# Kernel tuning notes

Hardware: AMD Instinct MI355X
Metric: run time of the kernel (lower is better)

## Reference

```python
import jax, jax.numpy as jnp
import numpy as np

B, N, DIM = 1, 65536, 256
H, D, G = 8, 64, 64  # heads, dim_head, slice_num


def setup_inputs() -> dict:
    key = jax.random.key(0)
    ks = jax.random.split(key, 16)
    s = 0.02
    return {
        "x": jax.random.normal(ks[0], (B, N, DIM), jnp.float32),
        "Wx": jax.random.normal(ks[1], (H * D, DIM), jnp.float32) * s,
        "bx": jnp.zeros((H * D,), jnp.float32),
        "Wt1": jax.random.normal(ks[2], (G, D), jnp.float32) * s,
        "bt1": jnp.zeros((G,), jnp.float32),
        "Wt2": jax.random.normal(ks[3], (1, G), jnp.float32) * s,
        "bt2": jnp.zeros((1,), jnp.float32),
        "bias": jnp.ones((1, H, 1, 1), jnp.float32) * 0.5,
        "Ws": jax.random.normal(ks[4], (G, D), jnp.float32) * s,
        "bs": jnp.zeros((G,), jnp.float32),
        "Wq": jax.random.normal(ks[5], (D, D), jnp.float32) * s,
        "Wk": jax.random.normal(ks[6], (D, D), jnp.float32) * s,
        "Wv": jax.random.normal(ks[7], (D, D), jnp.float32) * s,
        "Wout": jax.random.normal(ks[8], (DIM, H * D), jnp.float32) * s,
        "bout": jnp.zeros((DIM,), jnp.float32),
        "u": jax.random.uniform(ks[9], (B, H, N, G), jnp.float32),
    }


def _gelu(t):
    return jax.nn.gelu(t, approximate=False)  # torch default exact GELU


def reference(x, Wx, bx, Wt1, bt1, Wt2, bt2, bias, Ws, bs, Wq, Wk, Wv, Wout, bout, u):
    b, n, _ = x.shape
    h, d, g = Wt1.shape[1] and bias.shape[1], Wq.shape[0], Ws.shape[0]
    # project and split heads: b n (h d) -> b h n d
    x_mid = (x @ Wx.T + bx).reshape(b, n, h, d).transpose(0, 2, 1, 3)
    # per-point temperature MLP + learned bias, clamped
    temp = _gelu(_gelu(x_mid @ Wt1.T + bt1) @ Wt2.T + bt2) + bias  # (b,h,n,1)
    temp = jnp.maximum(temp, 0.01)
    # gumbel-softmax slice routing (soft, hard=False)
    logits = x_mid @ Ws.T + bs  # (b,h,n,g)
    gnoise = -jnp.log(-jnp.log(u + 1e-8) + 1e-8)
    slice_weights = jax.nn.softmax((logits + gnoise) / temp, axis=-1)
    norm = slice_weights.sum(axis=2)  # (b,h,g)
    # gather-aggregate points into g slice tokens
    slice_tokens = jnp.einsum('bhnc,bhng->bhgc', x_mid, slice_weights)
    slice_tokens = slice_tokens / (norm[..., None] + 1e-5)
    # tiny g x g attention among slice tokens
    q = slice_tokens @ Wq.T
    k = slice_tokens @ Wk.T
    v = slice_tokens @ Wv.T
    attn = jax.nn.softmax((q @ k.transpose(0, 1, 3, 2)) * (d ** -0.5), axis=-1)
    out_slice = attn @ v  # (b,h,g,d)
    # scatter-combine back to points
    out = jnp.einsum('bhgd,bhng->bhnd', out_slice, slice_weights)
    out = out.transpose(0, 2, 1, 3).reshape(b, n, h * d)
    return out @ Wout.T + bout
```

## Files before the change

kernel.cpp:

```cpp
#include <hip/hip_runtime.h>
#include <math.h>

#define NPTS  65536
#define DIMX  256
#define NH    8
#define HDIM  512

typedef __attribute__((ext_vector_type(4))) float f32x4;
typedef __attribute__((ext_vector_type(8))) short short8;
typedef __attribute__((ext_vector_type(8))) unsigned short ushort8;
typedef __attribute__((ext_vector_type(4))) unsigned short us4;

__device__ __forceinline__ ushort f2bf(float f) {
    unsigned x = __float_as_uint(f);
    return (ushort)((x + 0x7fffu + ((x >> 16) & 1u)) >> 16);
}
__device__ __forceinline__ float bf2f(ushort u) {
    return __uint_as_float((unsigned)u << 16);
}
__device__ __forceinline__ float erf_fast(float x) {
    float ax = fabsf(x);
    float t  = __builtin_amdgcn_rcpf(1.0f + 0.3275911f * ax);
    float p  = fmaf(fmaf(fmaf(fmaf(1.061405429f, t, -1.453152027f), t,
                   1.421413741f), t, -0.284496736f), t, 0.254829592f) * t;
    float y  = 1.0f - p * __expf(-ax * ax);
    return copysignf(y, x);
}
__device__ __forceinline__ float gelu_fast(float x) {
    return 0.5f * x * (1.0f + erf_fast(x * 0.7071067811865476f));
}

__global__ __launch_bounds__(256)
void prep_wb_kernel(const float* __restrict__ Ws, const float* __restrict__ Wt1,
                    ushort* __restrict__ wb) {
    const int t = threadIdx.x;
    #pragma unroll
    for (int i = 0; i < 32; ++i) {
        int idx = i * 256 + t;
        int row = idx >> 6, col = idx & 63;
        float v = (row < 64) ? Ws[row * 64 + col] : Wt1[(row - 64) * 64 + col];
        wb[idx] = f2bf(v);
    }
}

__global__ __launch_bounds__(256)
void gemm_xmid_kernel(const float* __restrict__ A, const float* __restrict__ B,
                      const float* __restrict__ bias, ushort* __restrict__ C) {
    __shared__ __align__(16) ushort Al[128][64];
    __shared__ __align__(16) ushort Bl[128][64];
    const int m0 = blockIdx.x * 128, n0 = blockIdx.y * 128;
    const int t = threadIdx.x, l = t & 63, w = t >> 6;
    const int wr = w >> 1, wc = w & 1;
    const int lr = l & 15, lq = l >> 4;

    f32x4 acc[4][4];
    #pragma unroll
    for (int mi = 0; mi < 4; ++mi)
        #pragma unroll
        for (int ni = 0; ni < 4; ++ni) acc[mi][ni] = (f32x4){0.f, 0.f, 0.f, 0.f};

    for (int ks = 0; ks < 4; ++ks) {
        __syncthreads();
        #pragma unroll
        for (int i = 0; i < 4; ++i) {
            int idx = i * 256 + t;
            int row = idx >> 3, g = idx & 7;
            const float* ap = &A[(size_t)(m0 + row) * 256 + ks * 64 + g * 8];
            float4 a0 = *(const float4*)ap;
            float4 a1 = *(const float4*)(ap + 4);
            ushort8 av = { f2bf(a0.x), f2bf(a0.y), f2bf(a0.z), f2bf(a0.w),
                           f2bf(a1.x), f2bf(a1.y), f2bf(a1.z), f2bf(a1.w) };
            *(ushort8*)&Al[row][(g ^ (row & 7)) * 8] = av;
            const float* bp = &B[(size_t)(n0 + row) * 256 + ks * 64 + g * 8];
            float4 b0 = *(const float4*)bp;
            float4 b1 = *(const float4*)(bp + 4);
            ushort8 bv = { f2bf(b0.x), f2bf(b0.y), f2bf(b0.z), f2bf(b0.w),
                           f2bf(b1.x), f2bf(b1.y), f2bf(b1.z), f2bf(b1.w) };
            *(ushort8*)&Bl[row][(g ^ (row & 7)) * 8] = bv;
        }
        __syncthreads();
        #pragma unroll
        for (int kf = 0; kf < 2; ++kf) {
            short8 af[4], bfr[4];
            #pragma unroll
            for (int mi = 0; mi < 4; ++mi) {
                int row = wr * 64 + mi * 16 + lr, g = kf * 4 + lq;
                af[mi] = *(const short8*)&Al[row][(g ^ (row & 7)) * 8];
            }
            #pragma unroll
            for (int ni = 0; ni < 4; ++ni) {
                int row = wc * 64 + ni * 16 + lr, g = kf * 4 + lq;
                bfr[ni] = *(const short8*)&Bl[row][(g ^ (row & 7)) * 8];
            }
            #pragma unroll
            for (int mi = 0; mi < 4; ++mi)
                #pragma unroll
                for (int ni = 0; ni < 4; ++ni)
                    acc[mi][ni] = __builtin_amdgcn_mfma_f32_16x16x32_bf16(
                        af[mi], bfr[ni], acc[mi][ni], 0, 0, 0);
        }
    }
    #pragma unroll
    for (int ni = 0; ni < 4; ++ni) {
        int col = n0 + wc * 64 + ni * 16 + lr;
        float bb = bias[col];
        #pragma unroll
        for (int mi = 0; mi < 4; ++mi)
            #pragma unroll
            for (int j = 0; j < 4; ++j) {
                int row = m0 + wr * 64 + mi * 16 + lq * 4 + j;
                C[(size_t)row * 512 + col] = f2bf(acc[mi][ni][j] + bb);
            }
    }
}

__global__ __launch_bounds__(256)
void lgt1_mfma_kernel(const ushort* __restrict__ xmb,
                      const ushort* __restrict__ wb,
                      const float* __restrict__ bs,  const float* __restrict__ bt1,
                      const float* __restrict__ Wt2, const float* __restrict__ bt2,
                      const float* __restrict__ biasp,
                      const float* __restrict__ u,
                      ushort* __restrict__ swb) {
    __shared__ __align__(16) ushort Al[128][64];
    const int h = blockIdx.y, m0 = blockIdx.x * 128;
    const int t = threadIdx.x, l = t & 63, w = t >> 6;
    const int lr = l & 15, lq = l >> 4;
    const float LOG2E = 1.4426950408889634f;
    const float LN2   = 0.6931471805599453f;
    const float SH2   = 36.0673760222f;

    #pragma unroll
    for (int i = 0; i < 4; ++i) {
        int idx = i * 256 + t;
        int row = idx >> 3, g = idx & 7;
        ushort8 av = *(const ushort8*)&xmb[(size_t)(m0 + row) * 512 + h * 64 + g * 8];
        *(ushort8*)&Al[row][(g ^ (row & 7)) * 8] = av;
    }

    float uu0[4][4];
    #pragma unroll
    for (int jj = 0; jj < 4; ++jj) {
        const int n = m0 + w * 32 + lq * 4 + jj;
        const float* up = &u[((size_t)h * NPTS + n) * 64 + lr];
        #pragma unroll
        for (int ni = 0; ni < 4; ++ni) uu0[jj][ni] = up[ni * 16];
    }
    __syncthreads();

    f32x4 acc[2][8];
    #pragma unroll
    for (int mi = 0; mi < 2; ++mi)
        #pragma unroll
        for (int ni = 0; ni < 8; ++ni) acc[mi][ni] = (f32x4){0.f, 0.f, 0.f, 0.f};

    #pragma unroll
    for (int kf = 0; kf < 2; ++kf) {
        const int g = kf * 4 + lq;
        short8 af[2], bfr[8];
        #pragma unroll
        for (int mi = 0; mi < 2; ++mi) {
            int row = w * 32 + mi * 16 + lr;
            af[mi] = *(const short8*)&Al[row][(g ^ (row & 7)) * 8];
        }
        #pragma unroll
        for (int ni = 0; ni < 8; ++ni)
            bfr[ni] = *(const short8*)&wb[(size_t)(ni * 16 + lr) * 64 + g * 8];
        #pragma unroll
        for (int mi = 0; mi < 2; ++mi)
            #pragma unroll
            for (int ni = 0; ni < 8; ++ni)
                acc[mi][ni] = __builtin_amdgcn_mfma_f32_16x16x32_bf16(
                    af[mi], bfr[ni], acc[mi][ni], 0, 0, 0);
    }

    float uu1[4][4];
    #pragma unroll
    for (int jj = 0; jj < 4; ++jj) {
        const int n = m0 + w * 32 + 16 + lq * 4 + jj;
        const float* up = &u[((size_t)h * NPTS + n) * 64 + lr];
        #pragma unroll
        for (int ni = 0; ni < 4; ++ni) uu1[jj][ni] = up[ni * 16];
    }

    const float bt2v = bt2[0], biasph = biasp[h];
    float bsr[4], bt1r[4], wt2r[4];
    #pragma unroll
    for (int ni = 0; ni < 4; ++ni) {
        bsr[ni]  = bs [ni * 16 + lr];
        bt1r[ni] = bt1[ni * 16 + lr];
        wt2r[ni] = Wt2[ni * 16 + lr];
    }

    #pragma unroll
    for (int mi = 0; mi < 2; ++mi) {
        float ts[4];
        #pragma unroll
        for (int jj = 0; jj < 4; ++jj) {
            float s = 0.f;
            #pragma unroll
            for (int ni = 0; ni < 4; ++ni)
                s += gelu_fast(acc[mi][ni + 4][jj] + bt1r[ni]) * wt2r[ni];
            ts[jj] = s;
        }
        #pragma unroll
        for (int off = 1; off <= 8; off <<= 1) {
            #pragma unroll
            for (int jj = 0; jj < 4; ++jj) ts[jj] += __shfl_xor(ts[jj], off);
        }
        float invt[4], invt2[4];
        #pragma unroll
        for (int jj = 0; jj < 4; ++jj) {
            float tmp = gelu_fast(ts[jj] + bt2v) + biasph;
            tmp = fmaxf(tmp, 0.01f);
            invt[jj]  = __builtin_amdgcn_rcpf(tmp);
            invt2[jj] = invt[jj] * LOG2E;
        }
        float sv[4][4], ps[4] = {0.f, 0.f, 0.f, 0.f};
        #pragma unroll
        for (int jj = 0; jj < 4; ++jj) {
            #pragma unroll
            for (int ni = 0; ni < 4; ++ni) {
                float uuv = (mi == 0 ? uu0[jj][ni] : uu1[jj][ni]);
                float L1 = __log2f(uuv + 1e-8f);
                float inner = fmaf(-LN2, L1, 1e-8f);
                float L2v = __log2f(inner);
                float base = fmaf(acc[mi][ni][jj] + bsr[ni], invt2[jj], -SH2);
                sv[jj][ni] = __builtin_amdgcn_exp2f(fmaf(-invt[jj], L2v, base));
                ps[jj] += sv[jj][ni];
            }
        }
        #pragma unroll
        for (int off = 1; off <= 8; off <<= 1) {
            #pragma unroll
            for (int jj = 0; jj < 4; ++jj) ps[jj] += __shfl_xor(ps[jj], off);
        }
        #pragma unroll
        for (int jj = 0; jj < 4; ++jj) {
            const int n = m0 + w * 32 + mi * 16 + lq * 4 + jj;
            const float inv = __builtin_amdgcn_rcpf(ps[jj]);
            ushort* sp = &swb[(size_t)n * 512 + h * 64 + lr];
            #pragma unroll
            for (int ni = 0; ni < 4; ++ni)
                sp[ni * 16] = f2bf(sv[jj][ni] * inv);
        }
    }
}

__global__ __launch_bounds__(256)
void gather_mfma_kernel(const ushort* __restrict__ xmb, const ushort* __restrict__ swb,
                        float* __restrict__ stp, float* __restrict__ normp) {
    __shared__ __align__(16) ushort swT[64][128];
    __shared__ __align__(16) ushort xT [64][128];
    const int h  = blockIdx.y;
    const int n0 = blockIdx.x * 1024;
    const int t  = threadIdx.x, l = t & 63, w = t >> 6;
    const int lr = l & 15, lq = l >> 4;
    const int gb = t & 7;
    const int ng = t >> 3;

    f32x4 acc[4][4];
    #pragma unroll
    for (int gi = 0; gi < 4; ++gi)
        #pragma unroll
        for (int ci = 0; ci < 4; ++ci) acc[gi][ci] = (f32x4){0.f, 0.f, 0.f, 0.f};
    float nrm8[8];
    #pragma unroll
    for (int j = 0; j < 8; ++j) nrm8[j] = 0.f;

    for (int r = 0; r < 8; ++r) {
        const int nt = n0 + r * 128;
        ushort8 sv[4], xv[4];
        #pragma unroll
        for (int i = 0; i < 4; ++i) {
            int n = nt + ng * 4 + i;
            sv[i] = *(const ushort8*)&swb[(size_t)n * 512 + h * 64 + gb * 8];
            xv[i] = *(const ushort8*)&xmb[(size_t)n * 512 + h * 64 + gb * 8];
        }
        __syncthreads();
        #pragma unroll
        for (int j = 0; j < 8; ++j) {
            int g   = gb * 8 + j;
            int swz = (ng >> 1) ^ (g & 7) ^ ((g >> 3) & 7);
            int off = swz * 8 + (ng & 1) * 4;
            us4 s4 = { sv[0][j], sv[1][j], sv[2][j], sv[3][j] };
            us4 x4 = { xv[0][j], xv[1][j], xv[2][j], xv[3][j] };
            *(us4*)&swT[g][off] = s4;
            *(us4*)&xT [g][off] = x4;
            nrm8[j] += (bf2f(sv[0][j]) + bf2f(sv[1][j]))
                     + (bf2f(sv[2][j]) + bf2f(sv[3][j]));
        }
        __syncthreads();
        short8 af[4], bfr[4];
        #pragma unroll
        for (int gi = 0; gi < 4; ++gi) {
            int g   = gi * 16 + lr;
            int swz = (w * 4 + lq) ^ (g & 7) ^ ((g >> 3) & 7);
            af[gi]  = *(const short8*)&swT[g][swz * 8];
            bfr[gi] = *(const short8*)&xT [g][swz * 8];
        }
        #pragma unroll
        for (int gi = 0; gi < 4; ++gi)
            #pragma unroll
            for (int ci = 0; ci < 4; ++ci)
                acc[gi][ci] = __builtin_amdgcn_mfma_f32_16x16x32_bf16(
                    af[gi], bfr[ci], acc[gi][ci], 0, 0, 0);
    }

    const size_t base = ((size_t)h * 256 + blockIdx.x * 4 + w) * 4096;
    #pragma unroll
    for (int gi = 0; gi < 4; ++gi)
        #pragma unroll
        for (int ci = 0; ci < 4; ++ci)
            #pragma unroll
            for (int j = 0; j < 4; ++j)
                stp[base + (size_t)(gi * 16 + lq * 4 + j) * 64 + ci * 16 + lr]
                    = acc[gi][ci][j];

    __syncthreads();
    float* narr = (float*)swT;
    #pragma unroll
    for (int j = 0; j < 8; ++j) narr[ng * 64 + gb * 8 + j] = nrm8[j];
    __syncthreads();
    if (t < 64) {
        float s = 0.f;
        #pragma unroll 8
        for (int k = 0; k < 32; ++k) s += narr[k * 64 + t];
        normp[((size_t)h * 64 + blockIdx.x) * 64 + t] = s;
    }
}

__global__ __launch_bounds__(256)
void reduce_st_kernel(const float* __restrict__ stp, const float* __restrict__ normp,
                      float* __restrict__ st_red, float* __restrict__ nrm) {
    const int h = blockIdx.x;
    const int e = blockIdx.y * 256 + threadIdx.x;
    float s = 0.f;
    #pragma unroll 8
    for (int ch = 0; ch < 256; ++ch)
        s += stp[((size_t)h * 256 + ch) * 4096 + e];
    st_red[(size_t)h * 4096 + e] = s;
    if (blockIdx.y == 0 && threadIdx.x < 64) {
        float ns = 0.f;
        #pragma unroll 8
        for (int ch = 0; ch < 64; ++ch)
            ns += normp[((size_t)h * 64 + ch) * 64 + threadIdx.x];
        nrm[h * 64 + threadIdx.x] = ns + 1e-5f;
    }
}

__global__ __launch_bounds__(256)
void attn_small_kernel(const float* __restrict__ st_red, const float* __restrict__ nrm,
                       const float* __restrict__ Wq, const float* __restrict__ Wk,
                       const float* __restrict__ Wv, float* __restrict__ osl) {
    __shared__ float st[64][68];
    __shared__ float ql[64][68];
    __shared__ float kl[64][68];
    __shared__ float vl[64][68];
    __shared__ float sc[64][68];
    __shared__ float nl[64];
    const int h = blockIdx.x;
    const int t = threadIdx.x;

    if (t < 64) nl[t] = nrm[h * 64 + t];
    __syncthreads();
    for (int e = t; e < 4096; e += 256)
        st[e>>6][e&63] = st_red[(size_t)h * 4096 + e] / nl[e>>6];
    __syncthreads();
    for (int e = t; e < 4096; e += 256) {
        int g = e >> 6, dd = e & 63;
        float aq = 0.f, ak = 0.f, av = 0.f;
        for (int cc = 0; cc < 64; ++cc) {
            float sv = st[g][cc];
            aq = fmaf(sv, Wq[dd*64 + cc], aq);
            ak = fmaf(sv, Wk[dd*64 + cc], ak);
            av = fmaf(sv, Wv[dd*64 + cc], av);
        }
        ql[g][dd] = aq; kl[g][dd] = ak; vl[g][dd] = av;
    }
    __syncthreads();
    for (int e = t; e < 4096; e += 256) {
        int g = e >> 6, gp = e & 63;
        float s = 0.f;
        for (int dd = 0; dd < 64; ++dd) s = fmaf(ql[g][dd], kl[gp][dd], s);
        sc[g][gp] = s * 0.125f;
    }
    __syncthreads();
    if (t < 64) {
        float m = -1e30f;
        for (int j = 0; j < 64; ++j) m = fmaxf(m, sc[t][j]);
        float ssum = 0.f;
        for (int j = 0; j < 64; ++j) { float p = expf(sc[t][j] - m); sc[t][j] = p; ssum += p; }
        float inv = 1.f / ssum;
        for (int j = 0; j < 64; ++j) sc[t][j] *= inv;
    }
    __syncthreads();
    for (int e = t; e < 4096; e += 256) {
        int g = e >> 6, dd = e & 63;
        float s = 0.f;
        for (int gp = 0; gp < 64; ++gp) s = fmaf(sc[g][gp], vl[gp][dd], s);
        osl[(size_t)h * 4096 + e] = s;
    }
}

__global__ __launch_bounds__(256)
void fold_kernel(const float* __restrict__ osl, const float* __restrict__ Wout,
                 float* __restrict__ Mt) {
    __shared__ float os[64][65];
    __shared__ float wl[128][65];
    const int h  = blockIdx.x;
    const int i0 = blockIdx.y * 128;
    const int t  = threadIdx.x;
    for (int e = t; e < 4096; e += 256) os[e>>6][e&63] = osl[(size_t)h * 4096 + e];
    for (int e = t; e < 8192; e += 256) {
        int i = e >> 6, d = e & 63;
        wl[i][d] = Wout[(size_t)(i0 + i) * HDIM + h * 64 + d];
    }
    __syncthreads();
    const int g = t & 63, iq = t >> 6;
    #pragma unroll 4
    for (int k = 0; k < 32; ++k) {
        int i = iq * 32 + k;
        float s = 0.f;
        #pragma unroll
        for (int d = 0; d < 64; ++d) s = fmaf(os[g][d], wl[i][d], s);
        Mt[(size_t)(i0 + i) * HDIM + h * 64 + g] = s;
    }
}

__global__ __launch_bounds__(256)
void gemm_out_kernel(const ushort* __restrict__ A, const float* __restrict__ B,
                     const float* __restrict__ bias, float* __restrict__ C) {
    __shared__ __align__(16) ushort Al[128][64];
    __shared__ __align__(16) ushort Bl[128][64];
    const int m0 = blockIdx.x * 128, n0 = blockIdx.y * 128;
    const int t = threadIdx.x, l = t & 63, w = t >> 6;
    const int wr = w >> 1, wc = w & 1;
    const int lr = l & 15, lq = l >> 4;

    f32x4 acc[4][4];
    #pragma unroll
    for (int mi = 0; mi < 4; ++mi)
        #pragma unroll
        for (int ni = 0; ni < 4; ++ni) acc[mi][ni] = (f32x4){0.f, 0.f, 0.f, 0.f};

    for (int ks = 0; ks < 8; ++ks) {
        __syncthreads();
        #pragma unroll
        for (int i = 0; i < 4; ++i) {
            int idx = i * 256 + t;
            int row = idx >> 3, g = idx & 7;
            ushort8 av = *(const ushort8*)&A[(size_t)(m0 + row) * 512 + ks * 64 + g * 8];
            *(ushort8*)&Al[row][(g ^ (row & 7)) * 8] = av;
            const float* bp = &B[(size_t)(n0 + row) * 512 + ks * 64 + g * 8];
            float4 b0 = *(const float4*)bp;
            float4 b1 = *(const float4*)(bp + 4);
            ushort8 bv = { f2bf(b0.x), f2bf(b0.y), f2bf(b0.z), f2bf(b0.w),
                           f2bf(b1.x), f2bf(b1.y), f2bf(b1.z), f2bf(b1.w) };
            *(ushort8*)&Bl[row][(g ^ (row & 7)) * 8] = bv;
        }
        __syncthreads();
        #pragma unroll
        for (int kf = 0; kf < 2; ++kf) {
            short8 af[4], bfr[4];
            #pragma unroll
            for (int mi = 0; mi < 4; ++mi) {
                int row = wr * 64 + mi * 16 + lr, g = kf * 4 + lq;
                af[mi] = *(const short8*)&Al[row][(g ^ (row & 7)) * 8];
            }
            #pragma unroll
            for (int ni = 0; ni < 4; ++ni) {
                int row = wc * 64 + ni * 16 + lr, g = kf * 4 + lq;
                bfr[ni] = *(const short8*)&Bl[row][(g ^ (row & 7)) * 8];
            }
            #pragma unroll
            for (int mi = 0; mi < 4; ++mi)
                #pragma unroll
                for (int ni = 0; ni < 4; ++ni)
                    acc[mi][ni] = __builtin_amdgcn_mfma_f32_16x16x32_bf16(
                        af[mi], bfr[ni], acc[mi][ni], 0, 0, 0);
        }
    }
    #pragma unroll
    for (int ni = 0; ni < 4; ++ni) {
        int col = n0 + wc * 64 + ni * 16 + lr;
        float bb = bias[col];
        #pragma unroll
        for (int mi = 0; mi < 4; ++mi)
            #pragma unroll
            for (int j = 0; j < 4; ++j) {
                int row = m0 + wr * 64 + mi * 16 + lq * 4 + j;
                C[(size_t)row * 256 + col] = acc[mi][ni][j] + bb;
            }
    }
}

extern "C" void kernel_launch(void* const* d_in, const int* in_sizes, int n_in,
                              void* d_out, int out_size, void* d_ws, size_t ws_size,
                              hipStream_t stream) {
    const float* x    = (const float*)d_in[0];
    const float* Wx   = (const float*)d_in[1];
    const float* bx   = (const float*)d_in[2];
    const float* Wt1  = (const float*)d_in[3];
    const float* bt1  = (const float*)d_in[4];
    const float* Wt2  = (const float*)d_in[5];
    const float* bt2  = (const float*)d_in[6];
    const float* biasp= (const float*)d_in[7];
    const float* Ws   = (const float*)d_in[8];
    const float* bs   = (const float*)d_in[9];
    const float* Wq   = (const float*)d_in[10];
    const float* Wk   = (const float*)d_in[11];
    const float* Wv   = (const float*)d_in[12];
    const float* Wout = (const float*)d_in[13];
    const float* bout = (const float*)d_in[14];
    const float* u    = (const float*)d_in[15];
    float* out = (float*)d_out;

    float*  stp    = (float*)d_ws;
    float*  normp  = stp    + (size_t)NH * 256 * 4096;
    float*  Mt     = normp  + (size_t)NH * 64 * 64;
    float*  st_red = Mt     + (size_t)DIMX * HDIM;
    float*  nrm    = st_red + (size_t)NH * 4096;
    float*  osl    = nrm    + (size_t)NH * 64;
    ushort* wb     = (ushort*)(osl + (size_t)NH * 4096);
    ushort* xmb    = wb  + (size_t)128 * 64;
    ushort* swb    = xmb + (size_t)NPTS * HDIM;

    prep_wb_kernel<<<1, 256, 0, stream>>>(Ws, Wt1, wb);
    gemm_xmid_kernel<<<dim3(512, 4), 256, 0, stream>>>(x, Wx, bx, xmb);
    lgt1_mfma_kernel<<<dim3(512, 8), 256, 0, stream>>>(xmb, wb, bs, bt1,
                                                       Wt2, bt2, biasp, u, swb);
    gather_mfma_kernel<<<dim3(64, 8), 256, 0, stream>>>(xmb, swb, stp, normp);
    reduce_st_kernel<<<dim3(8, 16), 256, 0, stream>>>(stp, normp, st_red, nrm);
    attn_small_kernel<<<8, 256, 0, stream>>>(st_red, nrm, Wq, Wk, Wv, osl);
    fold_kernel<<<dim3(8, 2), 256, 0, stream>>>(osl, Wout, Mt);
    gemm_out_kernel<<<dim3(512, 2), 256, 0, stream>>>(swb, Mt, bout, out);
}
```

Before: 290.4 us.

## Pre-convert weights to bf16 and reduce gather partials in-block before writing

Wx is converted to bf16 once in an expanded prep kernel, and fold_kernel writes Mt as bf16. Both GEMMs can then load B tiles directly without per-tile fp32 loads and conversions. The gather kernel now sums its four per-wave partial slice-token tiles through shared memory before storing, which cuts the stp partial buffer and the reduce kernel's read traffic by a factor of four. This adds extra syncthreads and shared-memory passes in the gather epilogue, and rounds Mt to bf16 once instead of per tile, which gives the same values.

```diff
diff --git a/kernel.cpp b/kernel.cpp
--- a/kernel.cpp
+++ b/kernel.cpp
@@ -31,20 +31,32 @@
 }
 
 __global__ __launch_bounds__(256)
-void prep_wb_kernel(const float* __restrict__ Ws, const float* __restrict__ Wt1,
-                    ushort* __restrict__ wb) {
+void prep_kernel(const float* __restrict__ Wx, const float* __restrict__ Ws,
+                 const float* __restrict__ Wt1,
+                 ushort* __restrict__ Wxb, ushort* __restrict__ wb) {
     const int t = threadIdx.x;
-    #pragma unroll
-    for (int i = 0; i < 32; ++i) {
-        int idx = i * 256 + t;
+    if (blockIdx.x < 64) {
+        int idx = blockIdx.x * 2048 + t * 8;
+        float4 a0 = *(const float4*)&Wx[idx];
+        float4 a1 = *(const float4*)&Wx[idx + 4];
+        ushort8 v = { f2bf(a0.x), f2bf(a0.y), f2bf(a0.z), f2bf(a0.w),
+                      f2bf(a1.x), f2bf(a1.y), f2bf(a1.z), f2bf(a1.w) };
+        *(ushort8*)&Wxb[idx] = v;
+    } else {
+        int idx = (blockIdx.x - 64) * 2048 + t * 8;
         int row = idx >> 6, col = idx & 63;
-        float v = (row < 64) ? Ws[row * 64 + col] : Wt1[(row - 64) * 64 + col];
-        wb[idx] = f2bf(v);
-    }
-}
-
-__global__ __launch_bounds__(256)
-void gemm_xmid_kernel(const float* __restrict__ A, const float* __restrict__ B,
+        const float* src = (row < 64) ? &Ws[row * 64 + col]
+                                      : &Wt1[(row - 64) * 64 + col];
+        float4 a0 = *(const float4*)src;
+        float4 a1 = *(const float4*)(src + 4);
+        ushort8 v = { f2bf(a0.x), f2bf(a0.y), f2bf(a0.z), f2bf(a0.w),
+                      f2bf(a1.x), f2bf(a1.y), f2bf(a1.z), f2bf(a1.w) };
+        *(ushort8*)&wb[idx] = v;
+    }
+}
+
+__global__ __launch_bounds__(256)
+void gemm_xmid_kernel(const float* __restrict__ A, const ushort* __restrict__ B,
                       const float* __restrict__ bias, ushort* __restrict__ C) {
     __shared__ __align__(16) ushort Al[128][64];
     __shared__ __align__(16) ushort Bl[128][64];
@@ -71,11 +83,7 @@
             ushort8 av = { f2bf(a0.x), f2bf(a0.y), f2bf(a0.z), f2bf(a0.w),
                            f2bf(a1.x), f2bf(a1.y), f2bf(a1.z), f2bf(a1.w) };
             *(ushort8*)&Al[row][(g ^ (row & 7)) * 8] = av;
-            const float* bp = &B[(size_t)(n0 + row) * 256 + ks * 64 + g * 8];
-            float4 b0 = *(const float4*)bp;
-            float4 b1 = *(const float4*)(bp + 4);
-            ushort8 bv = { f2bf(b0.x), f2bf(b0.y), f2bf(b0.z), f2bf(b0.w),
-                           f2bf(b1.x), f2bf(b1.y), f2bf(b1.z), f2bf(b1.w) };
+            ushort8 bv = *(const ushort8*)&B[(size_t)(n0 + row) * 256 + ks * 64 + g * 8];
             *(ushort8*)&Bl[row][(g ^ (row & 7)) * 8] = bv;
         }
         __syncthreads();
@@ -250,8 +258,9 @@
 __global__ __launch_bounds__(256)
 void gather_mfma_kernel(const ushort* __restrict__ xmb, const ushort* __restrict__ swb,
                         float* __restrict__ stp, float* __restrict__ normp) {
-    __shared__ __align__(16) ushort swT[64][128];
-    __shared__ __align__(16) ushort xT [64][128];
+    __shared__ __align__(16) ushort tile[2][64][128];
+    ushort (* __restrict__ swT)[128] = tile[0];
+    ushort (* __restrict__ xT )[128] = tile[1];
     const int h  = blockIdx.y;
     const int n0 = blockIdx.x * 1024;
     const int t  = threadIdx.x, l = t & 63, w = t >> 6;
@@ -307,18 +316,32 @@
                     af[gi], bfr[ci], acc[gi][ci], 0, 0, 0);
     }
 
-    const size_t base = ((size_t)h * 256 + blockIdx.x * 4 + w) * 4096;
-    #pragma unroll
-    for (int gi = 0; gi < 4; ++gi)
-        #pragma unroll
-        for (int ci = 0; ci < 4; ++ci)
-            #pragma unroll
-            for (int j = 0; j < 4; ++j)
-                stp[base + (size_t)(gi * 16 + lq * 4 + j) * 64 + ci * 16 + lr]
-                    = acc[gi][ci][j];
-
-    __syncthreads();
-    float* narr = (float*)swT;
+    float* sred = (float*)tile;
+    const size_t stbase = ((size_t)h * 64 + blockIdx.x) * 4096;
+    #pragma unroll
+    for (int half = 0; half < 2; ++half) {
+        __syncthreads();
+        #pragma unroll
+        for (int gg = 0; gg < 2; ++gg) {
+            int gi = half * 2 + gg;
+            #pragma unroll
+            for (int ci = 0; ci < 4; ++ci)
+                #pragma unroll
+                for (int j = 0; j < 4; ++j)
+                    sred[(w * 32 + gg * 16 + lq * 4 + j) * 64 + ci * 16 + lr]
+                        = acc[gi][ci][j];
+        }
+        __syncthreads();
+        #pragma unroll
+        for (int i = 0; i < 8; ++i) {
+            int e = i * 256 + t;
+            float s = (sred[e] + sred[2048 + e]) + (sred[4096 + e] + sred[6144 + e]);
+            stp[stbase + half * 2048 + e] = s;
+        }
+    }
+
+    __syncthreads();
+    float* narr = (float*)tile;
     #pragma unroll
     for (int j = 0; j < 8; ++j) narr[ng * 64 + gb * 8 + j] = nrm8[j];
     __syncthreads();
@@ -337,8 +360,8 @@
     const int e = blockIdx.y * 256 + threadIdx.x;
     float s = 0.f;
     #pragma unroll 8
-    for (int ch = 0; ch < 256; ++ch)
-        s += stp[((size_t)h * 256 + ch) * 4096 + e];
+    for (int ch = 0; ch < 64; ++ch)
+        s += stp[((size_t)h * 64 + ch) * 4096 + e];
     st_red[(size_t)h * 4096 + e] = s;
     if (blockIdx.y == 0 && threadIdx.x < 64) {
         float ns = 0.f;
@@ -405,7 +428,7 @@
 
 __global__ __launch_bounds__(256)
 void fold_kernel(const float* __restrict__ osl, const float* __restrict__ Wout,
-                 float* __restrict__ Mt) {
+                 ushort* __restrict__ Mtb) {
     __shared__ float os[64][65];
     __shared__ float wl[128][65];
     const int h  = blockIdx.x;
@@ -424,12 +447,12 @@
         float s = 0.f;
         #pragma unroll
         for (int d = 0; d < 64; ++d) s = fmaf(os[g][d], wl[i][d], s);
-        Mt[(size_t)(i0 + i) * HDIM + h * 64 + g] = s;
-    }
-}
-
-__global__ __launch_bounds__(256)
-void gemm_out_kernel(const ushort* __restrict__ A, const float* __restrict__ B,
+        Mtb[(size_t)(i0 + i) * HDIM + h * 64 + g] = f2bf(s);
+    }
+}
+
+__global__ __launch_bounds__(256)
+void gemm_out_kernel(const ushort* __restrict__ A, const ushort* __restrict__ B,
                      const float* __restrict__ bias, float* __restrict__ C) {
     __shared__ __align__(16) ushort Al[128][64];
     __shared__ __align__(16) ushort Bl[128][64];
@@ -452,11 +475,7 @@
             int row = idx >> 3, g = idx & 7;
             ushort8 av = *(const ushort8*)&A[(size_t)(m0 + row) * 512 + ks * 64 + g * 8];
             *(ushort8*)&Al[row][(g ^ (row & 7)) * 8] = av;
-            const float* bp = &B[(size_t)(n0 + row) * 512 + ks * 64 + g * 8];
-            float4 b0 = *(const float4*)bp;
-            float4 b1 = *(const float4*)(bp + 4);
-            ushort8 bv = { f2bf(b0.x), f2bf(b0.y), f2bf(b0.z), f2bf(b0.w),
-                           f2bf(b1.x), f2bf(b1.y), f2bf(b1.z), f2bf(b1.w) };
+            ushort8 bv = *(const ushort8*)&B[(size_t)(n0 + row) * 512 + ks * 64 + g * 8];
             *(ushort8*)&Bl[row][(g ^ (row & 7)) * 8] = bv;
         }
         __syncthreads();
@@ -517,22 +536,23 @@
     float* out = (float*)d_out;
 
     float*  stp    = (float*)d_ws;
-    float*  normp  = stp    + (size_t)NH * 256 * 4096;
-    float*  Mt     = normp  + (size_t)NH * 64 * 64;
-    float*  st_red = Mt     + (size_t)DIMX * HDIM;
+    float*  normp  = stp    + (size_t)NH * 64 * 4096;
+    float*  st_red = normp  + (size_t)NH * 64 * 64;
     float*  nrm    = st_red + (size_t)NH * 4096;
     float*  osl    = nrm    + (size_t)NH * 64;
     ushort* wb     = (ushort*)(osl + (size_t)NH * 4096);
-    ushort* xmb    = wb  + (size_t)128 * 64;
+    ushort* Wxb    = wb  + (size_t)128 * 64;
+    ushort* Mtb    = Wxb + (size_t)HDIM * DIMX;
+    ushort* xmb    = Mtb + (size_t)DIMX * HDIM;
     ushort* swb    = xmb + (size_t)NPTS * HDIM;
 
-    prep_wb_kernel<<<1, 256, 0, stream>>>(Ws, Wt1, wb);
-    gemm_xmid_kernel<<<dim3(512, 4), 256, 0, stream>>>(x, Wx, bx, xmb);
+    prep_kernel<<<68, 256, 0, stream>>>(Wx, Ws, Wt1, Wxb, wb);
+    gemm_xmid_kernel<<<dim3(512, 4), 256, 0, stream>>>(x, Wxb, bx, xmb);
     lgt1_mfma_kernel<<<dim3(512, 8), 256, 0, stream>>>(xmb, wb, bs, bt1,
                                                        Wt2, bt2, biasp, u, swb);
     gather_mfma_kernel<<<dim3(64, 8), 256, 0, stream>>>(xmb, swb, stp, normp);
     reduce_st_kernel<<<dim3(8, 16), 256, 0, stream>>>(stp, normp, st_red, nrm);
     attn_small_kernel<<<8, 256, 0, stream>>>(st_red, nrm, Wq, Wk, Wv, osl);
-    fold_kernel<<<dim3(8, 2), 256, 0, stream>>>(osl, Wout, Mt);
-    gemm_out_kernel<<<dim3(512, 2), 256, 0, stream>>>(swb, Mt, bout, out);
-}
+    fold_kernel<<<dim3(8, 2), 256, 0, stream>>>(osl, Wout, Mtb);
+    gemm_out_kernel<<<dim3(512, 2), 256, 0, stream>>>(swb, Mtb, bout, out);
+}
```

After: 266.0 us. -8.4%, faster.
